# Kernel tuning notes

Measured on AMD Instinct MI355X. Metric: run time of the kernel, lower is better.

## Reference

```python
import jax, jax.numpy as jnp
import numpy as np

EMBED_DIM = 512
NUM_HEADS = 8
HEAD_DIM = EMBED_DIM // NUM_HEADS
SCALE = 1.0 / HEAD_DIM ** 0.5


def setup_inputs() -> dict:
    key = jax.random.key(0)
    ks = jax.random.split(key, 7)
    B, C, H, W = 8, EMBED_DIM, 32, 32
    x = jax.random.normal(ks[0], (B, C, H, W), dtype=jnp.float32)
    s = 1.0 / np.sqrt(EMBED_DIM)
    return {
        "x": x,
        "ln_gamma": jnp.ones((EMBED_DIM,), jnp.float32),
        "ln_beta": jnp.zeros((EMBED_DIM,), jnp.float32),
        "w_qkv": jax.random.uniform(ks[1], (EMBED_DIM, 3 * EMBED_DIM), jnp.float32, -s, s),
        "b_qkv": jax.random.uniform(ks[2], (3 * EMBED_DIM,), jnp.float32, -s, s),
        "w_proj": jax.random.uniform(ks[3], (EMBED_DIM, EMBED_DIM), jnp.float32, -s, s),
        "b_proj": jax.random.uniform(ks[4], (EMBED_DIM,), jnp.float32, -s, s),
    }


def reference(x, ln_gamma, ln_beta, w_qkv, b_qkv, w_proj, b_proj):
    B, C, H, W = x.shape
    N = H * W
    # LayerNorm over channel dim (applied in NHWC layout in the original)
    xs = x.reshape(B, C, N).transpose(0, 2, 1)  # [B, N, C]
    mu = jnp.mean(xs, axis=-1, keepdims=True)
    var = jnp.mean(jnp.square(xs - mu), axis=-1, keepdims=True)
    xn = (xs - mu) / jnp.sqrt(var + 1e-5) * ln_gamma + ln_beta
    # QKV projection
    qkv = xn @ w_qkv + b_qkv                        # [B, N, 3C]
    qkv = qkv.reshape(B, N, 3, NUM_HEADS, HEAD_DIM)
    q = qkv[:, :, 0].transpose(0, 2, 1, 3)         # [B, h, N, d]
    k = qkv[:, :, 1].transpose(0, 2, 1, 3)
    v = qkv[:, :, 2].transpose(0, 2, 1, 3)
    # Scaled dot-product attention (full N x N scores, as in source)
    attn = jnp.einsum('bhnd,bhmd->bhnm', q, k) * SCALE
    attn = jax.nn.softmax(attn, axis=-1)
    o = jnp.einsum('bhnm,bhmd->bhnd', attn, v)     # [B, h, N, d]
    o = o.transpose(0, 2, 1, 3).reshape(B, N, C)
    # Output projection (dropout is identity in eval)
    o = o @ w_proj + b_proj
    return o.transpose(0, 2, 1).reshape(B, C, H, W)
```

## Files before the change

### kernel.cpp

```cpp
#include <hip/hip_runtime.h>
#include <hip/hip_bf16.h>
#include <math.h>

#define B_   8
#define C_   512
#define NH_  8
#define HD_  64
#define NSP  1024
#define M_   (B_*NSP)
#define NQKV 1536
#define SCALE_ 0.125f
#define S2L_  0.18033688f

typedef __attribute__((ext_vector_type(8))) __bf16 bf16x8;
typedef __attribute__((ext_vector_type(4))) float  f32x4;

__device__ __forceinline__ unsigned short f2bf(float f) {
  unsigned int u = __float_as_uint(f);
  u = u + 0x7fffu + ((u >> 16) & 1u);
  return (unsigned short)(u >> 16);
}

__device__ __forceinline__ unsigned int pk2bf(float a, float b) {
  __hip_bfloat162 t = __float22bfloat162_rn(make_float2(a, b));
  unsigned int u; __builtin_memcpy(&u, &t, 4);
  return u;
}

__device__ __forceinline__ void async16(const unsigned short* g, unsigned short* l) {
  __builtin_amdgcn_global_load_lds(
      (const __attribute__((address_space(1))) void*)g,
      (__attribute__((address_space(3))) void*)l, 16, 0, 0);
}

__global__ void ln_stats_kernel(const float* __restrict__ x,
                                float* __restrict__ mean,
                                float* __restrict__ rstd) {
  int tx = threadIdx.x & 31, ty = threadIdx.x >> 5;
  int bx = blockIdx.x;
  int b  = bx >> 5;
  int n0 = (bx & 31) * 32;
  const float* xp = x + (size_t)b * C_ * NSP + n0 + tx;
  float s = 0.f, s2 = 0.f;
  for (int c = ty; c < C_; c += 8) {
    float v = xp[(size_t)c * NSP];
    s += v; s2 += v * v;
  }
  __shared__ float sh_s[8][32], sh_s2[8][32];
  sh_s[ty][tx] = s; sh_s2[ty][tx] = s2;
  __syncthreads();
  if (ty == 0) {
    float S = 0.f, S2 = 0.f;
    for (int j = 0; j < 8; j++) { S += sh_s[j][tx]; S2 += sh_s2[j][tx]; }
    float mu  = S * (1.0f / C_);
    float var = S2 * (1.0f / C_) - mu * mu;
    mean[b * NSP + n0 + tx] = mu;
    rstd[b * NSP + n0 + tx] = rsqrtf(var + 1e-5f);
  }
}

__global__ __launch_bounds__(256) void applyw_kernel(
    const float* __restrict__ x, const float* __restrict__ mean,
    const float* __restrict__ rstd, const float* __restrict__ gamma,
    const float* __restrict__ beta, const float* __restrict__ wqkv,
    const float* __restrict__ wproj, unsigned short* __restrict__ xn,
    unsigned short* __restrict__ wqkvT, unsigned short* __restrict__ wprojT) {
  int tid = threadIdx.x;
  __shared__ float tile[64][65];
  int tx = tid & 63, ty = tid >> 6;
  if (blockIdx.x >= 1024) {
    const float* W; unsigned short* WT; int NW, t;
    if (blockIdx.x < 1216) { W = wqkv;  WT = wqkvT;  NW = NQKV; t = blockIdx.x - 1024; }
    else                   { W = wproj; WT = wprojT; NW = C_;   t = blockIdx.x - 1216; }
    int ntiles = NW >> 6;
    int kt = t / ntiles, nt = t - kt * ntiles;
    for (int i = ty; i < 64; i += 4)
      tile[i][tx] = W[(size_t)(kt * 64 + i) * NW + nt * 64 + tx];
    __syncthreads();
    for (int i = ty; i < 64; i += 4)
      WT[(size_t)(nt * 64 + i) * C_ + kt * 64 + tx] = f2bf(tile[tx][i]);
    return;
  }
  int c0 = (blockIdx.x & 7) * 64;
  int n0 = ((blockIdx.x >> 3) & 15) * 64;
  int b  = blockIdx.x >> 7;
  const float* xp = x + ((size_t)b * C_ + c0) * NSP + n0;
  for (int i = ty; i < 64; i += 4)
    tile[i][tx] = xp[(size_t)i * NSP + tx];
  __syncthreads();
  float g = gamma[c0 + tx], be = beta[c0 + tx];
  unsigned short* op = xn + ((size_t)(b * NSP + n0)) * C_ + c0 + tx;
  for (int i = ty; i < 64; i += 4) {
    float mu = mean[b * NSP + n0 + i], rs = rstd[b * NSP + n0 + i];
    float v = (tile[tx][i] - mu) * rs * g + be;
    op[(size_t)i * C_] = f2bf(v);
  }
}

__global__ __launch_bounds__(256) void gemm_qkv_kernel(
    const unsigned short* __restrict__ A,
    const unsigned short* __restrict__ Bt,
    const float* __restrict__ bias,
    unsigned short* __restrict__ out0, unsigned short* __restrict__ out1) {
  __shared__ __align__(16) char smem[20480];
  unsigned short* As = (unsigned short*)smem;
  unsigned short* Bs = (unsigned short*)(smem + 8192);
  int tid = threadIdx.x;
  int wave = tid >> 6, lane = tid & 63, quad = lane >> 4, l15 = lane & 15;
  int n0 = blockIdx.x * 128, m0 = blockIdx.y * 128;
  int mrow = (wave >> 1) * 64, ncol = (wave & 1) * 64;
  int srow = lane >> 2, schunk = (lane & 3) * 8;
  f32x4 acc[4][4] = {};
  for (int k0 = 0; k0 < 512; k0 += 32) {
    if (k0) __syncthreads();
#pragma unroll
    for (int j = 0; j < 2; j++) {
      int r0 = (wave + 4 * j) * 16;
      async16(A + (size_t)(m0 + r0 + srow) * 512 + k0 + schunk, As + r0 * 32 + lane * 8);
      async16(Bt + (size_t)(n0 + r0 + srow) * 512 + k0 + schunk, Bs + r0 * 32 + lane * 8);
    }
    __syncthreads();
    bf16x8 a[4], bb[4];
#pragma unroll
    for (int mt = 0; mt < 4; mt++)
      a[mt] = *(const bf16x8*)(As + (mrow + mt * 16 + l15) * 32 + quad * 8);
#pragma unroll
    for (int nt = 0; nt < 4; nt++)
      bb[nt] = *(const bf16x8*)(Bs + (ncol + nt * 16 + l15) * 32 + quad * 8);
#pragma unroll
    for (int mt = 0; mt < 4; mt++)
#pragma unroll
      for (int nt = 0; nt < 4; nt++)
        acc[mt][nt] = __builtin_amdgcn_mfma_f32_16x16x32_bf16(
            a[mt], bb[nt], acc[mt][nt], 0, 0, 0);
  }
  if (n0 < 1024) {
    float sc = ((n0 + ncol) < 512) ? S2L_ : 1.0f;
#pragma unroll
    for (int mt = 0; mt < 4; mt++)
#pragma unroll
      for (int nt = 0; nt < 4; nt++)
#pragma unroll
        for (int r = 0; r < 4; r++) {
          int row = m0 + mrow + mt * 16 + quad * 4 + r;
          int col = n0 + ncol + nt * 16 + l15;
          out0[(size_t)row * 1024 + col] = f2bf((acc[mt][nt][r] + bias[col]) * sc);
        }
  } else {
    __syncthreads();
    unsigned short* buf = (unsigned short*)smem + wave * (64 * 17);
    int b = m0 >> 10, nbase = m0 & 1023;
    for (int nc = 0; nc < 4; nc++) {
#pragma unroll
      for (int mt = 0; mt < 4; mt++)
#pragma unroll
        for (int r = 0; r < 4; r++) {
          int col = n0 + ncol + nc * 16 + l15;
          buf[(mt * 16 + quad * 4 + r) * 17 + l15] = f2bf(acc[mt][nc][r] + bias[col]);
        }
      __syncthreads();
      for (int cc = 0; cc < 16; cc++) {
        int crel = n0 - 1024 + ncol + nc * 16 + cc;
        out1[((size_t)b * C_ + crel) * NSP + nbase + mrow + lane] = buf[lane * 17 + cc];
      }
      __syncthreads();
    }
  }
}

__global__ __launch_bounds__(256) void gemm_proj_kernel(
    const unsigned short* __restrict__ A,
    const unsigned short* __restrict__ Bt,
    const float* __restrict__ bias,
    float* __restrict__ O) {
  __shared__ __align__(16) char smem[20480];
  unsigned short* As = (unsigned short*)smem;
  unsigned short* Bs = (unsigned short*)(smem + 4096);
  int tid = threadIdx.x;
  int wave = tid >> 6, lane = tid & 63, quad = lane >> 4, l15 = lane & 15;
  int n0 = blockIdx.x * 128, m0 = blockIdx.y * 64;
  int wm0 = (wave >> 1) * 32, wc0 = (wave & 1) * 64;
  int srow = lane >> 2, schunk = (lane & 3) * 8;
  f32x4 acc[2][4] = {};
  for (int k0 = 0; k0 < 512; k0 += 32) {
    if (k0) __syncthreads();
    async16(A + (size_t)(m0 + wave * 16 + srow) * 512 + k0 + schunk,
            As + (wave * 16) * 32 + lane * 8);
#pragma unroll
    for (int j = 0; j < 2; j++) {
      int r0 = (wave + 4 * j) * 16;
      async16(Bt + (size_t)(n0 + r0 + srow) * 512 + k0 + schunk, Bs + r0 * 32 + lane * 8);
    }
    __syncthreads();
    bf16x8 a[2], bb[4];
#pragma unroll
    for (int mt = 0; mt < 2; mt++)
      a[mt] = *(const bf16x8*)(As + (wm0 + mt * 16 + l15) * 32 + quad * 8);
#pragma unroll
    for (int nt = 0; nt < 4; nt++)
      bb[nt] = *(const bf16x8*)(Bs + (wc0 + nt * 16 + l15) * 32 + quad * 8);
#pragma unroll
    for (int mt = 0; mt < 2; mt++)
#pragma unroll
      for (int nt = 0; nt < 4; nt++)
        acc[mt][nt] = __builtin_amdgcn_mfma_f32_16x16x32_bf16(
            a[mt], bb[nt], acc[mt][nt], 0, 0, 0);
  }
  __syncthreads();
  float* buf = (float*)smem + wave * (32 * 17);
  int b = m0 >> 10, nbase = m0 & 1023;
  for (int nc = 0; nc < 4; nc++) {
#pragma unroll
    for (int mt = 0; mt < 2; mt++)
#pragma unroll
      for (int r = 0; r < 4; r++) {
        int col = n0 + wc0 + nc * 16 + l15;
        buf[(mt * 16 + quad * 4 + r) * 17 + l15] = acc[mt][nc][r] + bias[col];
      }
#pragma unroll
    for (int j = 0; j < 8; j++) {
      int cl = j * 2 + (lane >> 5);
      int ml = lane & 31;
      int c = n0 + wc0 + nc * 16 + cl;
      O[((size_t)b * C_ + c) * NSP + nbase + wm0 + ml] = buf[ml * 17 + cl];
    }
  }
}

__global__ __launch_bounds__(256, 3) void attn_kernel(
    const unsigned short* __restrict__ qk,
    const unsigned short* __restrict__ vt,
    unsigned short* __restrict__ o_ws) {
  __shared__ __align__(16) unsigned short Ks[2][64][64];
  __shared__ __align__(16) unsigned short Vts[2][64][64];
  __shared__ __align__(16) unsigned short Ps[4][32][68];
  int tid = threadIdx.x;
  int wave = tid >> 6, lane = tid & 63, quad = lane >> 4, l15 = lane & 15;
  int qw = wave & 1, kh = wave >> 1;
  int b = blockIdx.x >> 3, h = blockIdx.x & 7;
  int q0 = blockIdx.y * 64 + qw * 32;
  int srow = lane >> 3, scc = lane & 7, swz = scc ^ srow;
  uint4 ones4 = (l15 == 0) ? make_uint4(0x3F803F80u, 0x3F803F80u, 0x3F803F80u, 0x3F803F80u)
                           : make_uint4(0u, 0u, 0u, 0u);
  bf16x8 av5; __builtin_memcpy(&av5, &ones4, 16);
  bf16x8 bq[2][2];
#pragma unroll
  for (int mt = 0; mt < 2; mt++)
#pragma unroll
    for (int ks = 0; ks < 2; ks++)
      bq[mt][ks] = *(const bf16x8*)(
          qk + (size_t)(b * NSP + q0 + mt * 16 + l15) * 1024 +
          h * 64 + ks * 32 + quad * 8);
  f32x4 ot[4][2] = {};
  f32x4 lacc[2] = {};
  for (int it = 0; it < 8; it++) {
    int k0 = kh * 512 + it * 64;
    __syncthreads();
#pragma unroll
    for (int g = 0; g < 4; g++) {
      int row = qw * 32 + g * 8;
      async16(qk + (size_t)(b * NSP + k0 + row + srow) * 1024 + 512 + h * 64 + swz * 8,
              &Ks[kh][row][0]);
      async16(vt + ((size_t)(b * C_ + h * 64 + row + srow)) * NSP + k0 + swz * 8,
              &Vts[kh][row][0]);
    }
    __syncthreads();
    bf16x8 ak[4][2];
#pragma unroll
    for (int n4 = 0; n4 < 4; n4++)
#pragma unroll
      for (int ks = 0; ks < 2; ks++)
        ak[n4][ks] = *(const bf16x8*)(
            &Ks[kh][n4 * 16 + l15][((ks * 4 + quad) ^ (l15 & 7)) * 8]);
    f32x4 s[4][2] = {};
#pragma unroll
    for (int n4 = 0; n4 < 4; n4++)
#pragma unroll
      for (int mt = 0; mt < 2; mt++)
#pragma unroll
        for (int ks = 0; ks < 2; ks++)
          s[n4][mt] = __builtin_amdgcn_mfma_f32_16x16x32_bf16(
              ak[n4][ks], bq[mt][ks], s[n4][mt], 0, 0, 0);
#pragma unroll
    for (int mt = 0; mt < 2; mt++)
#pragma unroll
      for (int n4 = 0; n4 < 4; n4++) {
        float p0 = __builtin_amdgcn_exp2f(s[n4][mt][0]);
        float p1 = __builtin_amdgcn_exp2f(s[n4][mt][1]);
        float p2 = __builtin_amdgcn_exp2f(s[n4][mt][2]);
        float p3 = __builtin_amdgcn_exp2f(s[n4][mt][3]);
        *(uint2*)(&Ps[wave][mt * 16 + l15][n4 * 16 + quad * 4]) =
            make_uint2(pk2bf(p0, p1), pk2bf(p2, p3));
      }
    bf16x8 av[4][2], bp[2][2];
#pragma unroll
    for (int dt = 0; dt < 4; dt++)
#pragma unroll
      for (int ks = 0; ks < 2; ks++)
        av[dt][ks] = *(const bf16x8*)(
            &Vts[kh][dt * 16 + l15][((ks * 4 + quad) ^ (l15 & 7)) * 8]);
#pragma unroll
    for (int mt = 0; mt < 2; mt++)
#pragma unroll
      for (int ks = 0; ks < 2; ks++)
        bp[mt][ks] = *(const bf16x8*)(&Ps[wave][mt * 16 + l15][ks * 32 + quad * 8]);
#pragma unroll
    for (int dt = 0; dt < 4; dt++)
#pragma unroll
      for (int mt = 0; mt < 2; mt++)
#pragma unroll
        for (int ks = 0; ks < 2; ks++)
          ot[dt][mt] = __builtin_amdgcn_mfma_f32_16x16x32_bf16(
              av[dt][ks], bp[mt][ks], ot[dt][mt], 0, 0, 0);
#pragma unroll
    for (int mt = 0; mt < 2; mt++)
#pragma unroll
      for (int ks = 0; ks < 2; ks++)
        lacc[mt] = __builtin_amdgcn_mfma_f32_16x16x32_bf16(
            av5, bp[mt][ks], lacc[mt], 0, 0, 0);
  }
  float* Cb = (float*)&Ks[0][0][0];
  float* Lb = (float*)&Vts[0][0][0];
#pragma unroll
  for (int mt = 0; mt < 2; mt++) {
    __syncthreads();
    if (kh == 1) {
#pragma unroll
      for (int dt = 0; dt < 4; dt++)
        *(f32x4*)&Cb[(qw * 16 + l15) * 68 + dt * 16 + quad * 4] = ot[dt][mt];
      if (quad == 0) Lb[qw * 16 + l15] = lacc[mt][0];
    }
    __syncthreads();
    if (kh == 0) {
#pragma unroll
      for (int dt = 0; dt < 4; dt++)
        ot[dt][mt] += *(const f32x4*)&Cb[(qw * 16 + l15) * 68 + dt * 16 + quad * 4];
      float lsum = lacc[mt][0] + Lb[qw * 16 + l15];
      float lv = __shfl(lsum, l15);
      float inv = 1.f / lv;
      size_t rowoff = (size_t)(b * NSP + q0 + mt * 16 + l15) * 512 + h * 64;
#pragma unroll
      for (int dt = 0; dt < 4; dt++)
        *(uint2*)(o_ws + rowoff + dt * 16 + quad * 4) =
            make_uint2(pk2bf(ot[dt][mt][0] * inv, ot[dt][mt][1] * inv),
                       pk2bf(ot[dt][mt][2] * inv, ot[dt][mt][3] * inv));
    }
  }
}

extern "C" void kernel_launch(void* const* d_in, const int* in_sizes, int n_in,
                              void* d_out, int out_size, void* d_ws, size_t ws_size,
                              hipStream_t stream) {
  const float* x     = (const float*)d_in[0];
  const float* gamma = (const float*)d_in[1];
  const float* beta  = (const float*)d_in[2];
  const float* wqkv  = (const float*)d_in[3];
  const float* bqkv  = (const float*)d_in[4];
  const float* wproj = (const float*)d_in[5];
  const float* bproj = (const float*)d_in[6];
  char* ws = (char*)d_ws;
  float*          mean   = (float*)ws;
  float*          rstd   = (float*)(ws + 32768);
  unsigned short* wqkvT  = (unsigned short*)(ws + 65536);
  unsigned short* wprojT = (unsigned short*)(ws + 1638400);
  unsigned short* qk_bf  = (unsigned short*)(ws + 2162688);
  unsigned short* vt_bf  = (unsigned short*)(ws + 18939904);
  unsigned short* xn_bf  = (unsigned short*)(ws + 27328512);
  unsigned short* o_bf   = xn_bf;
  float* out = (float*)d_out;

  ln_stats_kernel<<<256, 256, 0, stream>>>(x, mean, rstd);
  applyw_kernel<<<1024 + 192 + 64, 256, 0, stream>>>(x, mean, rstd, gamma, beta,
                                                     wqkv, wproj, xn_bf, wqkvT, wprojT);
  gemm_qkv_kernel<<<dim3(NQKV / 128, M_ / 128), 256, 0, stream>>>(
      xn_bf, wqkvT, bqkv, qk_bf, vt_bf);
  attn_kernel<<<dim3(B_ * NH_, NSP / 64), 256, 0, stream>>>(qk_bf, vt_bf, o_bf);
  gemm_proj_kernel<<<dim3(C_ / 128, M_ / 64), 256, 0, stream>>>(
      o_bf, wprojT, bproj, out);
}
```

Baseline: 174.3 us.

## Split LN stats across channel groups and double-buffer GEMM and attention loads

LN stats now run on four times as many blocks, each summing a quarter of the channels into partial buffers. The apply kernel combines the partials into per-row mean and rstd in shared memory. Both GEMMs get double-buffered LDS staging so the next K tile's async load overlaps the current MFMAs. Attention prefetches the next K/V tile into registers during compute and writes it to LDS afterwards. The cost is more LDS, more registers and an extra barrier per attention iteration, which may lower occupancy.

```diff
diff --git a/kernel.cpp b/kernel.cpp
--- a/kernel.cpp
+++ b/kernel.cpp
@@ -34,15 +34,16 @@
 }
 
 __global__ void ln_stats_kernel(const float* __restrict__ x,
-                                float* __restrict__ mean,
-                                float* __restrict__ rstd) {
+                                float* __restrict__ psum,
+                                float* __restrict__ psum2) {
   int tx = threadIdx.x & 31, ty = threadIdx.x >> 5;
-  int bx = blockIdx.x;
-  int b  = bx >> 5;
-  int n0 = (bx & 31) * 32;
+  int cg  = blockIdx.x & 3;
+  int nch = (blockIdx.x >> 2) & 31;
+  int b   = blockIdx.x >> 7;
+  int n0 = nch * 32;
   const float* xp = x + (size_t)b * C_ * NSP + n0 + tx;
   float s = 0.f, s2 = 0.f;
-  for (int c = ty; c < C_; c += 8) {
+  for (int c = cg * 128 + ty; c < cg * 128 + 128; c += 8) {
     float v = xp[(size_t)c * NSP];
     s += v; s2 += v * v;
   }
@@ -52,16 +53,14 @@
   if (ty == 0) {
     float S = 0.f, S2 = 0.f;
     for (int j = 0; j < 8; j++) { S += sh_s[j][tx]; S2 += sh_s2[j][tx]; }
-    float mu  = S * (1.0f / C_);
-    float var = S2 * (1.0f / C_) - mu * mu;
-    mean[b * NSP + n0 + tx] = mu;
-    rstd[b * NSP + n0 + tx] = rsqrtf(var + 1e-5f);
+    psum [cg * M_ + b * NSP + n0 + tx] = S;
+    psum2[cg * M_ + b * NSP + n0 + tx] = S2;
   }
 }
 
 __global__ __launch_bounds__(256) void applyw_kernel(
-    const float* __restrict__ x, const float* __restrict__ mean,
-    const float* __restrict__ rstd, const float* __restrict__ gamma,
+    const float* __restrict__ x, const float* __restrict__ psum,
+    const float* __restrict__ psum2, const float* __restrict__ gamma,
     const float* __restrict__ beta, const float* __restrict__ wqkv,
     const float* __restrict__ wproj, unsigned short* __restrict__ xn,
     unsigned short* __restrict__ wqkvT, unsigned short* __restrict__ wprojT) {
@@ -81,9 +80,19 @@
       WT[(size_t)(nt * 64 + i) * C_ + kt * 64 + tx] = f2bf(tile[tx][i]);
     return;
   }
+  __shared__ float smu[64], srs[64];
   int c0 = (blockIdx.x & 7) * 64;
   int n0 = ((blockIdx.x >> 3) & 15) * 64;
   int b  = blockIdx.x >> 7;
+  if (tid < 64) {
+    int n = b * NSP + n0 + tid;
+    float s  = psum [n] + psum [M_ + n] + psum [2 * M_ + n] + psum [3 * M_ + n];
+    float s2 = psum2[n] + psum2[M_ + n] + psum2[2 * M_ + n] + psum2[3 * M_ + n];
+    float mu = s * (1.0f / C_);
+    float var = s2 * (1.0f / C_) - mu * mu;
+    smu[tid] = mu;
+    srs[tid] = rsqrtf(var + 1e-5f);
+  }
   const float* xp = x + ((size_t)b * C_ + c0) * NSP + n0;
   for (int i = ty; i < 64; i += 4)
     tile[i][tx] = xp[(size_t)i * NSP + tx];
@@ -91,8 +100,7 @@
   float g = gamma[c0 + tx], be = beta[c0 + tx];
   unsigned short* op = xn + ((size_t)(b * NSP + n0)) * C_ + c0 + tx;
   for (int i = ty; i < 64; i += 4) {
-    float mu = mean[b * NSP + n0 + i], rs = rstd[b * NSP + n0 + i];
-    float v = (tile[tx][i] - mu) * rs * g + be;
+    float v = (tile[tx][i] - smu[i]) * srs[i] * g + be;
     op[(size_t)i * C_] = f2bf(v);
   }
 }
@@ -102,24 +110,30 @@
     const unsigned short* __restrict__ Bt,
     const float* __restrict__ bias,
     unsigned short* __restrict__ out0, unsigned short* __restrict__ out1) {
-  __shared__ __align__(16) char smem[20480];
-  unsigned short* As = (unsigned short*)smem;
-  unsigned short* Bs = (unsigned short*)(smem + 8192);
+  __shared__ __align__(16) char smem[32768];
   int tid = threadIdx.x;
   int wave = tid >> 6, lane = tid & 63, quad = lane >> 4, l15 = lane & 15;
   int n0 = blockIdx.x * 128, m0 = blockIdx.y * 128;
   int mrow = (wave >> 1) * 64, ncol = (wave & 1) * 64;
   int srow = lane >> 2, schunk = (lane & 3) * 8;
-  f32x4 acc[4][4] = {};
-  for (int k0 = 0; k0 < 512; k0 += 32) {
-    if (k0) __syncthreads();
+  auto stage = [&](int k0, int buf) {
+    unsigned short* As = (unsigned short*)(smem + buf * 16384);
+    unsigned short* Bs = (unsigned short*)(smem + buf * 16384 + 8192);
 #pragma unroll
     for (int j = 0; j < 2; j++) {
       int r0 = (wave + 4 * j) * 16;
       async16(A + (size_t)(m0 + r0 + srow) * 512 + k0 + schunk, As + r0 * 32 + lane * 8);
       async16(Bt + (size_t)(n0 + r0 + srow) * 512 + k0 + schunk, Bs + r0 * 32 + lane * 8);
     }
-    __syncthreads();
+  };
+  f32x4 acc[4][4] = {};
+  stage(0, 0);
+  for (int kt = 0; kt < 16; kt++) {
+    int cur = kt & 1;
+    __syncthreads();
+    if (kt < 15) stage((kt + 1) * 32, cur ^ 1);
+    unsigned short* As = (unsigned short*)(smem + cur * 16384);
+    unsigned short* Bs = (unsigned short*)(smem + cur * 16384 + 8192);
     bf16x8 a[4], bb[4];
 #pragma unroll
     for (int mt = 0; mt < 4; mt++)
@@ -173,17 +187,15 @@
     const unsigned short* __restrict__ Bt,
     const float* __restrict__ bias,
     float* __restrict__ O) {
-  __shared__ __align__(16) char smem[20480];
-  unsigned short* As = (unsigned short*)smem;
-  unsigned short* Bs = (unsigned short*)(smem + 4096);
+  __shared__ __align__(16) char smem[24576];
   int tid = threadIdx.x;
   int wave = tid >> 6, lane = tid & 63, quad = lane >> 4, l15 = lane & 15;
   int n0 = blockIdx.x * 128, m0 = blockIdx.y * 64;
   int wm0 = (wave >> 1) * 32, wc0 = (wave & 1) * 64;
   int srow = lane >> 2, schunk = (lane & 3) * 8;
-  f32x4 acc[2][4] = {};
-  for (int k0 = 0; k0 < 512; k0 += 32) {
-    if (k0) __syncthreads();
+  auto stage = [&](int k0, int buf) {
+    unsigned short* As = (unsigned short*)(smem + buf * 12288);
+    unsigned short* Bs = (unsigned short*)(smem + buf * 12288 + 4096);
     async16(A + (size_t)(m0 + wave * 16 + srow) * 512 + k0 + schunk,
             As + (wave * 16) * 32 + lane * 8);
 #pragma unroll
@@ -191,7 +203,15 @@
       int r0 = (wave + 4 * j) * 16;
       async16(Bt + (size_t)(n0 + r0 + srow) * 512 + k0 + schunk, Bs + r0 * 32 + lane * 8);
     }
-    __syncthreads();
+  };
+  f32x4 acc[2][4] = {};
+  stage(0, 0);
+  for (int kt = 0; kt < 16; kt++) {
+    int cur = kt & 1;
+    __syncthreads();
+    if (kt < 15) stage((kt + 1) * 32, cur ^ 1);
+    unsigned short* As = (unsigned short*)(smem + cur * 12288);
+    unsigned short* Bs = (unsigned short*)(smem + cur * 12288 + 4096);
     bf16x8 a[2], bb[4];
 #pragma unroll
     for (int mt = 0; mt < 2; mt++)
@@ -251,20 +271,28 @@
       bq[mt][ks] = *(const bf16x8*)(
           qk + (size_t)(b * NSP + q0 + mt * 16 + l15) * 1024 +
           h * 64 + ks * 32 + quad * 8);
+#pragma unroll
+  for (int g = 0; g < 4; g++) {
+    int row = qw * 32 + g * 8;
+    async16(qk + (size_t)(b * NSP + kh * 512 + row + srow) * 1024 + 512 + h * 64 + swz * 8,
+            &Ks[kh][row][0]);
+    async16(vt + ((size_t)(b * C_ + h * 64 + row + srow)) * NSP + kh * 512 + swz * 8,
+            &Vts[kh][row][0]);
+  }
   f32x4 ot[4][2] = {};
   f32x4 lacc[2] = {};
+  __syncthreads();
   for (int it = 0; it < 8; it++) {
-    int k0 = kh * 512 + it * 64;
-    __syncthreads();
-#pragma unroll
-    for (int g = 0; g < 4; g++) {
-      int row = qw * 32 + g * 8;
-      async16(qk + (size_t)(b * NSP + k0 + row + srow) * 1024 + 512 + h * 64 + swz * 8,
-              &Ks[kh][row][0]);
-      async16(vt + ((size_t)(b * C_ + h * 64 + row + srow)) * NSP + k0 + swz * 8,
-              &Vts[kh][row][0]);
-    }
-    __syncthreads();
+    uint4 kr[4], vr[4];
+    if (it < 7) {
+      int k0n = kh * 512 + (it + 1) * 64;
+#pragma unroll
+      for (int g = 0; g < 4; g++) {
+        int row = qw * 32 + g * 8 + srow;
+        kr[g] = *(const uint4*)(qk + (size_t)(b * NSP + k0n + row) * 1024 + 512 + h * 64 + swz * 8);
+        vr[g] = *(const uint4*)(vt + ((size_t)(b * C_ + h * 64 + row)) * NSP + k0n + swz * 8);
+      }
+    }
     bf16x8 ak[4][2];
 #pragma unroll
     for (int n4 = 0; n4 < 4; n4++)
@@ -318,6 +346,16 @@
       for (int ks = 0; ks < 2; ks++)
         lacc[mt] = __builtin_amdgcn_mfma_f32_16x16x32_bf16(
             av5, bp[mt][ks], lacc[mt], 0, 0, 0);
+    if (it < 7) {
+      __syncthreads();
+#pragma unroll
+      for (int g = 0; g < 4; g++) {
+        int row = qw * 32 + g * 8 + srow;
+        *(uint4*)(&Ks[kh][row][scc * 8]) = kr[g];
+        *(uint4*)(&Vts[kh][row][scc * 8]) = vr[g];
+      }
+      __syncthreads();
+    }
   }
   float* Cb = (float*)&Ks[0][0][0];
   float* Lb = (float*)&Vts[0][0][0];
@@ -359,18 +397,18 @@
   const float* wproj = (const float*)d_in[5];
   const float* bproj = (const float*)d_in[6];
   char* ws = (char*)d_ws;
-  float*          mean   = (float*)ws;
-  float*          rstd   = (float*)(ws + 32768);
-  unsigned short* wqkvT  = (unsigned short*)(ws + 65536);
-  unsigned short* wprojT = (unsigned short*)(ws + 1638400);
-  unsigned short* qk_bf  = (unsigned short*)(ws + 2162688);
-  unsigned short* vt_bf  = (unsigned short*)(ws + 18939904);
-  unsigned short* xn_bf  = (unsigned short*)(ws + 27328512);
+  float*          psum   = (float*)ws;
+  float*          psum2  = (float*)(ws + 131072);
+  unsigned short* wqkvT  = (unsigned short*)(ws + 262144);
+  unsigned short* wprojT = (unsigned short*)(ws + 1835008);
+  unsigned short* qk_bf  = (unsigned short*)(ws + 2359296);
+  unsigned short* vt_bf  = (unsigned short*)(ws + 19136512);
+  unsigned short* xn_bf  = (unsigned short*)(ws + 27525120);
   unsigned short* o_bf   = xn_bf;
   float* out = (float*)d_out;
 
-  ln_stats_kernel<<<256, 256, 0, stream>>>(x, mean, rstd);
-  applyw_kernel<<<1024 + 192 + 64, 256, 0, stream>>>(x, mean, rstd, gamma, beta,
+  ln_stats_kernel<<<1024, 256, 0, stream>>>(x, psum, psum2);
+  applyw_kernel<<<1024 + 192 + 64, 256, 0, stream>>>(x, psum, psum2, gamma, beta,
                                                      wqkv, wproj, xn_bf, wqkvT, wprojT);
   gemm_qkv_kernel<<<dim3(NQKV / 128, M_ / 128), 256, 0, stream>>>(
       xn_bf, wqkvT, bqkv, qk_bf, vt_bf);
```

Result: slower. 210.4 us (+20.8%).
